# Optimization experiments

Measured on AMD Instinct MI355X. Metric: run time of the kernel, lower is better.

Reference implementation:

```python
import jax, jax.numpy as jnp
import numpy as np
import math

B, T, EMB, HD = 4, 2048, 2048, 128
HALF = HD // 2


def setup_inputs() -> dict:
    key = jax.random.key(0)
    ks = jax.random.split(key, 4)
    x = jax.random.normal(ks[0], (B, T, EMB), dtype=jnp.float32)
    s = 1.0 / math.sqrt(EMB)
    Wq = jax.random.normal(ks[1], (EMB, HD), dtype=jnp.float32) * s
    Wk = jax.random.normal(ks[2], (EMB, HD), dtype=jnp.float32) * s
    Wv = jax.random.normal(ks[3], (EMB, HD), dtype=jnp.float32) * s
    # Standard RoPE rotation table: theta_i = 10000^(-2i/HD), angle = pos * theta
    inv_freq = 1.0 / (10000.0 ** (np.arange(0, HALF, dtype=np.float32) / HALF))
    angles = np.arange(T, dtype=np.float32)[:, None] * inv_freq[None, :]  # [T, HALF]
    rot_cos = jnp.asarray(np.cos(angles), dtype=jnp.float32)
    rot_sin = jnp.asarray(np.sin(angles), dtype=jnp.float32)
    # Additive causal mask: 0 on/below diagonal, -1e9 above
    NEG = -1e9
    mask = jnp.where(jnp.tril(jnp.ones((T, T), dtype=bool)), 0.0, NEG).astype(jnp.float32)
    return {"x": x, "Wq": Wq, "Wk": Wk, "Wv": Wv,
            "rot_cos": rot_cos, "rot_sin": rot_sin, "mask": mask}


def _apply_rope(q, rot_cos, rot_sin):
    # q: [B, T, HD]; view last dim as HALF complex pairs and rotate
    qp = q.reshape(q.shape[0], q.shape[1], HALF, 2)
    re, im = qp[..., 0], qp[..., 1]
    out_re = re * rot_cos - im * rot_sin  # broadcast [T,HALF] over batch
    out_im = re * rot_sin + im * rot_cos
    return jnp.stack([out_re, out_im], axis=-1).reshape(q.shape)


def reference(x, Wq, Wk, Wv, rot_cos, rot_sin, mask):
    Q = x @ Wq  # [B, T, HD]
    K = x @ Wk
    V = x @ Wv
    Q = _apply_rope(Q, rot_cos, rot_sin)
    K = _apply_rope(K, rot_cos, rot_sin)
    scores = jnp.einsum('bqd,bkd->bqk', Q, K) / math.sqrt(HD)
    probs = jax.nn.softmax(scores + mask, axis=-1)  # dropout is identity in eval
    return jnp.einsum('bqk,bkd->bqd', probs, V)
```

## Files before the change

kernel.cpp:

```cpp
#include <hip/hip_runtime.h>
#include <cstddef>
#include <cstdint>

#define T_SEQ 2048
#define EMB_D 2048
#define HD_D  128

typedef __attribute__((ext_vector_type(8))) short short8;
typedef __attribute__((ext_vector_type(4))) float f32x4;
typedef __attribute__((ext_vector_type(4))) unsigned short ushort4v;
typedef __attribute__((ext_vector_type(8))) unsigned short ushort8v;
typedef __attribute__((ext_vector_type(2))) unsigned int uint2v;

static __device__ __forceinline__ unsigned short f2bf_rne(float f) {
    union { float f; unsigned u; } v; v.f = f;
    unsigned r = v.u + 0x7fffu + ((v.u >> 16) & 1u);
    return (unsigned short)(r >> 16);
}
static __device__ __forceinline__ unsigned short f2bf_fast(float f) {
    union { float f; unsigned u; } v; v.f = f;
    return (unsigned short)((v.u + 0x8000u) >> 16);
}
static __device__ __forceinline__ float bf2f(unsigned short h) {
    union { unsigned u; float f; } v; v.u = ((unsigned)h) << 16;
    return v.f;
}
static __device__ __forceinline__ unsigned pk2(float a, float b) {
    union { float f; unsigned u; } x, y; x.f = a; y.f = b;
    return __builtin_amdgcn_perm(y.u + 0x8000u, x.u + 0x8000u, 0x07060302);
}
#define EXP2F(x) __builtin_amdgcn_exp2f(x)

__global__ __launch_bounds__(256) void prep_weights(
    const float* __restrict__ Wq, const float* __restrict__ Wk,
    const float* __restrict__ Wv, unsigned short* __restrict__ Wt)
{
    __shared__ __attribute__((aligned(16))) unsigned short tw[64 * 132];
    const int w = blockIdx.y;
    const int k0 = blockIdx.x * 64;
    const float* W = (w == 0) ? Wq : (w == 1) ? Wk : Wv;
    const int tid = threadIdx.x;
#pragma unroll
    for (int p = 0; p < 8; p++) {
        const int f = p * 256 + tid;
        const int row = f >> 5, c4 = f & 31;
        const float4 v = *(const float4*)&W[(size_t)(k0 + row) * HD_D + c4 * 4];
        ushort4v h = { f2bf_rne(v.x), f2bf_rne(v.y), f2bf_rne(v.z), f2bf_rne(v.w) };
        *(ushort4v*)&tw[row * 132 + c4 * 4] = h;
    }
    __syncthreads();
    const int kk = (tid & 7) * 8;
#pragma unroll
    for (int p = 0; p < 4; p++) {
        const int n = p * 32 + (tid >> 3);
        ushort8v o;
#pragma unroll
        for (int jj = 0; jj < 8; jj++) o[jj] = tw[(kk + jj) * 132 + n];
        *(ushort8v*)&Wt[(size_t)w * (HD_D * EMB_D) + (size_t)n * EMB_D + k0 + kk] = o;
    }
}

__global__ __launch_bounds__(512, 4) void qkv_fused(
    const float* __restrict__ x, const unsigned short* __restrict__ Wt,
    const float* __restrict__ rcos, const float* __restrict__ rsin,
    unsigned short* __restrict__ Qb, unsigned short* __restrict__ Kb,
    unsigned short* __restrict__ Vt)
{
    __shared__ __attribute__((aligned(16))) unsigned short xsm[2][32 * 64];
    __shared__ __attribute__((aligned(16))) unsigned short wsm[2][192 * 64];
    const int L = blockIdx.x;
    const int xcd = L & 7, s = L >> 3;
    const int cg = s & 1;
    const int m0 = (xcd * 32 + (s >> 1)) * 32;
    const int tid = threadIdx.x;
    const int lane = tid & 63, wave = tid >> 6;
    const int wm = wave >> 2, wn = wave & 3;
    const int l15 = lane & 15, lq = lane >> 4;

    const int xrow = tid >> 4, xc = tid & 15;
    const float* xsrc = x + (size_t)(m0 + xrow) * EMB_D + xc * 4;
    const int wrow = tid >> 3, wc = tid & 7;
    const unsigned short* wsrc = Wt + (size_t)(cg * 192 + wrow) * EMB_D + wc * 8;

    const int xw  = xrow * 128 + (((xc >> 1) ^ (xrow & 7)) << 4) + (xc & 1) * 8;
    const int wwo = wrow * 128 + ((wc ^ (wrow & 7)) << 4);

    int ra[2], rb[3][2];
#pragma unroll
    for (int ks = 0; ks < 2; ks++) {
        const int row = wm * 16 + l15;
        ra[ks] = row * 128 + (((ks * 4 + lq) ^ (row & 7)) << 4);
    }
#pragma unroll
    for (int jj = 0; jj < 3; jj++)
#pragma unroll
        for (int ks = 0; ks < 2; ks++) {
            const int row = wn * 48 + jj * 16 + l15;
            rb[jj][ks] = row * 128 + (((ks * 4 + lq) ^ (row & 7)) << 4);
        }

    f32x4 acc[3];
#pragma unroll
    for (int j = 0; j < 3; j++) acc[j] = (f32x4){0.f, 0.f, 0.f, 0.f};

    float4 xr[3];
    short8 wr[3][3];

#define LOADN(SET, K)                                                             \
    do {                                                                          \
        xr[SET] = *(const float4*)(xsrc + (K));                                   \
        _Pragma("unroll")                                                         \
        for (int p = 0; p < 3; p++)                                               \
            wr[SET][p] = *(const short8*)(wsrc + (size_t)p * (64 * EMB_D) + (K)); \
    } while (0)

#define STAGE(SET, BUF)                                                           \
    do {                                                                          \
        char* xb = (char*)&xsm[BUF][0];                                           \
        char* wb = (char*)&wsm[BUF][0];                                           \
        uint2v u;                                                                 \
        u.x = pk2(xr[SET].x, xr[SET].y);                                          \
        u.y = pk2(xr[SET].z, xr[SET].w);                                          \
        *(uint2v*)(xb + xw) = u;                                                  \
        _Pragma("unroll")                                                         \
        for (int p = 0; p < 3; p++)                                               \
            *(short8*)(wb + wwo + p * 8192) = wr[SET][p];                         \
    } while (0)

#define COMPUTE(BUF)                                                              \
    do {                                                                          \
        const char* xb = (const char*)&xsm[BUF][0];                               \
        const char* wb = (const char*)&wsm[BUF][0];                               \
        short8 Af[2];                                                             \
        _Pragma("unroll")                                                         \
        for (int ks = 0; ks < 2; ks++)                                            \
            Af[ks] = *(const short8*)(xb + ra[ks]);                               \
        __builtin_amdgcn_s_setprio(1);                                            \
        _Pragma("unroll")                                                         \
        for (int ks = 0; ks < 2; ks++)                                            \
            _Pragma("unroll")                                                     \
            for (int jj = 0; jj < 3; jj++) {                                      \
                const short8 Bf = *(const short8*)(wb + rb[jj][ks]);              \
                acc[jj] = __builtin_amdgcn_mfma_f32_16x16x32_bf16(                \
                    Af[ks], Bf, acc[jj], 0, 0, 0);                                \
            }                                                                     \
        __builtin_amdgcn_s_setprio(0);                                            \
    } while (0)

#define BARX() asm volatile("s_waitcnt lgkmcnt(0)\n\ts_barrier" ::: "memory")

    LOADN(0, 0);
    LOADN(1, 64);
    LOADN(2, 128);
    STAGE(0, 0);
    LOADN(0, 192);

#pragma clang loop unroll(disable)
    for (int j = 0; j < 24; j += 6) {
        BARX(); STAGE(1, 1); LOADN(1, (j + 4) * 64); COMPUTE(0);
        BARX(); STAGE(2, 0); LOADN(2, (j + 5) * 64); COMPUTE(1);
        BARX(); STAGE(0, 1); LOADN(0, (j + 6) * 64); COMPUTE(0);
        BARX(); STAGE(1, 0); LOADN(1, (j + 7) * 64); COMPUTE(1);
        BARX(); STAGE(2, 1); LOADN(2, (j + 8) * 64); COMPUTE(0);
        BARX(); STAGE(0, 0); LOADN(0, (j + 9) * 64); COMPUTE(1);
    }
    BARX(); STAGE(1, 1); LOADN(1, 28 * 64); COMPUTE(0);
    BARX(); STAGE(2, 0); LOADN(2, 29 * 64); COMPUTE(1);
    BARX(); STAGE(0, 1); LOADN(0, 30 * 64); COMPUTE(0);
    BARX(); STAGE(1, 0); LOADN(1, 31 * 64); COMPUTE(1);
    BARX(); STAGE(2, 1);                    COMPUTE(0);
    BARX(); STAGE(0, 0);                    COMPUTE(1);
    BARX(); STAGE(1, 1);                    COMPUTE(0);
    BARX();                                 COMPUTE(1);

#undef LOADN
#undef STAGE
#undef COMPUTE
#undef BARX

    const float qscale = 0.08838834764831845f * 1.4426950408889634f;
#pragma unroll
    for (int r = 0; r < 4; r++) {
        const int row = m0 + wm * 16 + lq * 4 + r;
        const int t = row & (T_SEQ - 1);
        const int bb = row >> 11;
#pragma unroll
        for (int j = 0; j < 3; j++) {
            const int col = cg * 192 + wn * 48 + j * 16 + l15;
            const int mat = col >> 7, mcol = col & 127;
            const float v = acc[j][r];
            if (mat == 2) {
                Vt[((size_t)bb * HD_D + mcol) * T_SEQ + t] = f2bf_rne(v);
            } else {
                const int ip = mcol >> 1;
                const float c = rcos[t * 64 + ip];
                const float s2 = rsin[t * 64 + ip];
                const float pv = __shfl_xor(v, 1);
                float rv = (mcol & 1) ? (pv * s2 + v * c) : (v * c - pv * s2);
                if (mat == 0) {
                    rv *= qscale;
                    Qb[(size_t)row * HD_D + mcol] = f2bf_rne(rv);
                } else {
                    Kb[(size_t)row * HD_D + mcol] = f2bf_rne(rv);
                }
            }
        }
    }
}

__global__ __launch_bounds__(256, 2) void attn(
    const unsigned short* __restrict__ Qb, const unsigned short* __restrict__ Kb,
    const unsigned short* __restrict__ Vt, float* __restrict__ O0,
    unsigned short* __restrict__ O1, float* __restrict__ Lp)
{
    __shared__ __attribute__((aligned(16))) unsigned short O_s[4][32 * 128];
    __shared__ __attribute__((aligned(16))) unsigned short P_s[4][32 * 40];
    __shared__ float l_s[4][32];

    const int tid = threadIdx.x;
    const int lane = tid & 63, wave = tid >> 6;
    const int l15 = lane & 15, lq = lane >> 4;
    const int kf = lq * 8;

    const int L = blockIdx.x;
    const int g = L & 1;
    const int b = (L >> 1) & 3;
    const int q0 = (63 - (L >> 3)) * 32;
    const int kend = q0 + 32;
    const float M2 = 16.0f;

    const unsigned short* Qp = Qb + (size_t)(b * T_SEQ + q0) * HD_D;
    short8 aQ[2][4];
#pragma unroll
    for (int i = 0; i < 2; i++)
#pragma unroll
        for (int d = 0; d < 4; d++)
            aQ[i][d] = *(const short8*)&Qp[(size_t)(i * 16 + l15) * HD_D + d * 32 + kf];

    f32x4 acc[2][8];
#pragma unroll
    for (int i = 0; i < 2; i++)
#pragma unroll
        for (int d = 0; d < 8; d++) acc[i][d] = (f32x4){0.f, 0.f, 0.f, 0.f};
    float l_r[2][4] = {{0.f, 0.f, 0.f, 0.f}, {0.f, 0.f, 0.f, 0.f}};

    const unsigned short* Kbase = Kb + (size_t)b * T_SEQ * HD_D;
    const unsigned short* Vbase = Vt + (size_t)b * HD_D * T_SEQ;
    unsigned short* Pw = &P_s[wave][0];

    for (int c = 2 * wave + g; c * 32 < kend; c += 8) {
        const int kA = c * 32;
        const unsigned short* Kp = Kbase + (size_t)kA * HD_D;
        short8 KA[8];
#pragma unroll
        for (int d = 0; d < 4; d++)
#pragma unroll
            for (int n = 0; n < 2; n++)
                KA[d * 2 + n] = *(const short8*)&Kp[(size_t)(n * 16 + l15) * HD_D + d * 32 + kf];

        f32x4 sc[2][2];
#pragma unroll
        for (int i = 0; i < 2; i++)
#pragma unroll
            for (int n = 0; n < 2; n++) sc[i][n] = (f32x4){0.f, 0.f, 0.f, 0.f};
#pragma unroll
        for (int d = 0; d < 4; d++)
#pragma unroll
            for (int i = 0; i < 2; i++)
#pragma unroll
                for (int n = 0; n < 2; n++)
                    sc[i][n] = __builtin_amdgcn_mfma_f32_16x16x32_bf16(
                        aQ[i][d], KA[d * 2 + n], sc[i][n], 0, 0, 0);

        short8 VA[8];
#pragma unroll
        for (int d = 0; d < 8; d++)
            VA[d] = *(const short8*)&Vbase[(size_t)(d * 16 + l15) * T_SEQ + kA + kf];

#pragma unroll
        for (int i = 0; i < 2; i++)
#pragma unroll
            for (int r = 0; r < 4; r++) {
                const int q = q0 + i * 16 + lq * 4 + r;
                const float p0 = ((kA + l15)      <= q) ? EXP2F(sc[i][0][r] - M2) : 0.f;
                const float p1 = ((kA + 16 + l15) <= q) ? EXP2F(sc[i][1][r] - M2) : 0.f;
                l_r[i][r] += p0 + p1;
                const int prow = (i * 16 + lq * 4 + r) * 40;
                Pw[prow + l15]      = f2bf_fast(p0);
                Pw[prow + 16 + l15] = f2bf_fast(p1);
            }
        short8 pA[2];
#pragma unroll
        for (int i = 0; i < 2; i++)
            pA[i] = *(const short8*)&Pw[(i * 16 + l15) * 40 + kf];
#pragma unroll
        for (int i = 0; i < 2; i++)
#pragma unroll
            for (int d = 0; d < 8; d++)
                acc[i][d] = __builtin_amdgcn_mfma_f32_16x16x32_bf16(pA[i], VA[d], acc[i][d], 0, 0, 0);
    }

#pragma unroll
    for (int i = 0; i < 2; i++)
#pragma unroll
        for (int r = 0; r < 4; r++) {
            float lr = l_r[i][r];
            lr += __shfl_xor(lr, 1);
            lr += __shfl_xor(lr, 2);
            lr += __shfl_xor(lr, 4);
            lr += __shfl_xor(lr, 8);
            if (l15 == 0) l_s[wave][i * 16 + lq * 4 + r] = lr;
#pragma unroll
            for (int d = 0; d < 8; d++)
                O_s[wave][(i * 16 + lq * 4 + r) * 128 + d * 16 + l15] = f2bf_fast(acc[i][d][r]);
        }
    __syncthreads();

#pragma unroll
    for (int pass = 0; pass < 2; pass++) {
        const int row = pass * 16 + (tid >> 4);
        const int dc = (tid & 15) * 8;
        const float lt = l_s[0][row] + l_s[1][row] + l_s[2][row] + l_s[3][row];
        float o[8];
#pragma unroll
        for (int k = 0; k < 8; k++) o[k] = 0.f;
#pragma unroll
        for (int w2 = 0; w2 < 4; w2++) {
            const ushort8v pv = *(const ushort8v*)&O_s[w2][row * 128 + dc];
#pragma unroll
            for (int k = 0; k < 8; k++) o[k] += bf2f(pv[k]);
        }
        const size_t grow = (size_t)(b * T_SEQ + q0 + row);
        if (g == 0) {
            float* op = O0 + grow * HD_D + dc;
#pragma unroll
            for (int k = 0; k < 8; k++) op[k] = o[k];
        } else {
            ushort8v h;
#pragma unroll
            for (int k = 0; k < 8; k++) h[k] = f2bf_fast(o[k]);
            *(ushort8v*)&O1[grow * HD_D + dc] = h;
        }
        if ((tid & 15) == 0) Lp[g * 8192 + grow] = lt;
    }
}

__global__ __launch_bounds__(256) void attn_merge(
    float* __restrict__ out, const unsigned short* __restrict__ O1,
    const float* __restrict__ Lp)
{
    const int idx = blockIdx.x * 256 + threadIdx.x;
    const int row = idx >> 5;
    f32x4 a = ((f32x4*)out)[idx];
    const ushort4v h = ((const ushort4v*)O1)[idx];
    f32x4 bv = { bf2f(h.x), bf2f(h.y), bf2f(h.z), bf2f(h.w) };
    const float inv = 1.0f / (Lp[row] + Lp[8192 + row]);
    ((f32x4*)out)[idx] = (a + bv) * inv;
}

extern "C" void kernel_launch(void* const* d_in, const int* in_sizes, int n_in,
                              void* d_out, int out_size, void* d_ws, size_t ws_size,
                              hipStream_t stream)
{
    (void)in_sizes; (void)n_in; (void)out_size; (void)ws_size;
    const float* x  = (const float*)d_in[0];
    const float* Wq = (const float*)d_in[1];
    const float* Wk = (const float*)d_in[2];
    const float* Wv = (const float*)d_in[3];
    const float* rc = (const float*)d_in[4];
    const float* rs = (const float*)d_in[5];
    float* out = (float*)d_out;

    char* ws = (char*)d_ws;
    unsigned short* Wt = (unsigned short*)(ws);
    unsigned short* Qb = (unsigned short*)(ws + 1572864);
    unsigned short* Kb = (unsigned short*)(ws + 3670016);
    unsigned short* Vt = (unsigned short*)(ws + 5767168);
    unsigned short* O1 = (unsigned short*)(ws + 7864320);
    float*          Lp = (float*)(ws + 9961472);

    prep_weights<<<dim3(32, 3), 256, 0, stream>>>(Wq, Wk, Wv, Wt);
    qkv_fused   <<<dim3(512),   512, 0, stream>>>(x, Wt, rc, rs, Qb, Kb, Vt);
    attn        <<<dim3(512),   256, 0, stream>>>(Qb, Kb, Vt, out, O1, Lp);
    attn_merge  <<<dim3(1024),  256, 0, stream>>>(out, O1, Lp);
}
```

Measured before the change: 173.5 us.

## Retile QKV projection to 64x96 block tiles with 128-wide K steps

The QKV projection now gives each block a 64-row by 96-column output tile (four column groups) instead of 32x192. Each of 4 waves computes 2x3 MFMA tiles, and the K step grows from 64 to 128, with double buffering replacing the triple-register pipeline. The aim is more MFMA work per LDS fragment load (A fragments reused across three B tiles, B across two A tiles) and fewer barriers. In exchange it uses more registers, fewer waves per block, and larger LDS use, which may lower occupancy.

```diff
diff --git a/kernel.cpp b/kernel.cpp
--- a/kernel.cpp
+++ b/kernel.cpp
@@ -60,148 +60,162 @@
     }
 }
 
-__global__ __launch_bounds__(512, 4) void qkv_fused(
+__global__ __launch_bounds__(256, 2) void qkv_fused(
     const float* __restrict__ x, const unsigned short* __restrict__ Wt,
     const float* __restrict__ rcos, const float* __restrict__ rsin,
     unsigned short* __restrict__ Qb, unsigned short* __restrict__ Kb,
     unsigned short* __restrict__ Vt)
 {
-    __shared__ __attribute__((aligned(16))) unsigned short xsm[2][32 * 64];
-    __shared__ __attribute__((aligned(16))) unsigned short wsm[2][192 * 64];
+    __shared__ __attribute__((aligned(16))) unsigned short xsm[2][64 * 128];
+    __shared__ __attribute__((aligned(16))) unsigned short wsm[2][96 * 128];
     const int L = blockIdx.x;
     const int xcd = L & 7, s = L >> 3;
-    const int cg = s & 1;
-    const int m0 = (xcd * 32 + (s >> 1)) * 32;
+    const int ng = s & 3;
+    const int m0 = (xcd * 16 + (s >> 2)) * 64;
     const int tid = threadIdx.x;
     const int lane = tid & 63, wave = tid >> 6;
-    const int wm = wave >> 2, wn = wave & 3;
+    const int wm = wave >> 1, wn = wave & 1;
     const int l15 = lane & 15, lq = lane >> 4;
 
-    const int xrow = tid >> 4, xc = tid & 15;
-    const float* xsrc = x + (size_t)(m0 + xrow) * EMB_D + xc * 4;
-    const int wrow = tid >> 3, wc = tid & 7;
-    const unsigned short* wsrc = Wt + (size_t)(cg * 192 + wrow) * EMB_D + wc * 8;
-
-    const int xw  = xrow * 128 + (((xc >> 1) ^ (xrow & 7)) << 4) + (xc & 1) * 8;
-    const int wwo = wrow * 128 + ((wc ^ (wrow & 7)) << 4);
-
-    int ra[2], rb[3][2];
-#pragma unroll
-    for (int ks = 0; ks < 2; ks++) {
-        const int row = wm * 16 + l15;
-        ra[ks] = row * 128 + (((ks * 4 + lq) ^ (row & 7)) << 4);
-    }
+    const int xrow = tid >> 5, xc4 = tid & 31;
+    const float* xsrc = x + (size_t)(m0 + xrow) * EMB_D + xc4 * 4;
+    const int wrow = tid >> 4, wc = tid & 15;
+    const unsigned short* wsrc = Wt + (size_t)(ng * 96 + wrow) * EMB_D + wc * 8;
+
+    const int xw  = xrow * 256 + (((xc4 >> 1) ^ (xrow & 7)) << 4) + (xc4 & 1) * 8;
+    const int wwo = wrow * 256 + ((wc ^ (wrow & 7)) << 4);
+
+    int ra[2][4], rb[3][4];
+#pragma unroll
+    for (int i = 0; i < 2; i++)
+#pragma unroll
+        for (int ks = 0; ks < 4; ks++) {
+            const int row = wm * 32 + i * 16 + l15;
+            ra[i][ks] = row * 256 + (((ks * 4 + lq) ^ (row & 7)) << 4);
+        }
 #pragma unroll
     for (int jj = 0; jj < 3; jj++)
 #pragma unroll
-        for (int ks = 0; ks < 2; ks++) {
+        for (int ks = 0; ks < 4; ks++) {
             const int row = wn * 48 + jj * 16 + l15;
-            rb[jj][ks] = row * 128 + (((ks * 4 + lq) ^ (row & 7)) << 4);
-        }
-
-    f32x4 acc[3];
-#pragma unroll
-    for (int j = 0; j < 3; j++) acc[j] = (f32x4){0.f, 0.f, 0.f, 0.f};
-
-    float4 xr[3];
-    short8 wr[3][3];
-
-#define LOADN(SET, K)                                                             \
-    do {                                                                          \
-        xr[SET] = *(const float4*)(xsrc + (K));                                   \
-        _Pragma("unroll")                                                         \
-        for (int p = 0; p < 3; p++)                                               \
-            wr[SET][p] = *(const short8*)(wsrc + (size_t)p * (64 * EMB_D) + (K)); \
+            rb[jj][ks] = row * 256 + (((ks * 4 + lq) ^ (row & 7)) << 4);
+        }
+
+    f32x4 acc[2][3];
+#pragma unroll
+    for (int i = 0; i < 2; i++)
+#pragma unroll
+        for (int j = 0; j < 3; j++) acc[i][j] = (f32x4){0.f, 0.f, 0.f, 0.f};
+
+    float4 xr[2][8];
+    short8 wr[6];
+
+#define LOADX(S, K)                                                              \
+    do {                                                                         \
+        _Pragma("unroll")                                                        \
+        for (int p = 0; p < 8; p++)                                              \
+            xr[S][p] = *(const float4*)(xsrc + (size_t)p * (8 * EMB_D) + (K));   \
     } while (0)
 
-#define STAGE(SET, BUF)                                                           \
-    do {                                                                          \
-        char* xb = (char*)&xsm[BUF][0];                                           \
-        char* wb = (char*)&wsm[BUF][0];                                           \
-        uint2v u;                                                                 \
-        u.x = pk2(xr[SET].x, xr[SET].y);                                          \
-        u.y = pk2(xr[SET].z, xr[SET].w);                                          \
-        *(uint2v*)(xb + xw) = u;                                                  \
-        _Pragma("unroll")                                                         \
-        for (int p = 0; p < 3; p++)                                               \
-            *(short8*)(wb + wwo + p * 8192) = wr[SET][p];                         \
+#define LOADW(K)                                                                 \
+    do {                                                                         \
+        _Pragma("unroll")                                                        \
+        for (int p = 0; p < 6; p++)                                              \
+            wr[p] = *(const short8*)(wsrc + (size_t)p * (16 * EMB_D) + (K));     \
     } while (0)
 
-#define COMPUTE(BUF)                                                              \
-    do {                                                                          \
-        const char* xb = (const char*)&xsm[BUF][0];                               \
-        const char* wb = (const char*)&wsm[BUF][0];                               \
-        short8 Af[2];                                                             \
-        _Pragma("unroll")                                                         \
-        for (int ks = 0; ks < 2; ks++)                                            \
-            Af[ks] = *(const short8*)(xb + ra[ks]);                               \
-        __builtin_amdgcn_s_setprio(1);                                            \
-        _Pragma("unroll")                                                         \
-        for (int ks = 0; ks < 2; ks++)                                            \
-            _Pragma("unroll")                                                     \
-            for (int jj = 0; jj < 3; jj++) {                                      \
-                const short8 Bf = *(const short8*)(wb + rb[jj][ks]);              \
-                acc[jj] = __builtin_amdgcn_mfma_f32_16x16x32_bf16(                \
-                    Af[ks], Bf, acc[jj], 0, 0, 0);                                \
-            }                                                                     \
-        __builtin_amdgcn_s_setprio(0);                                            \
+#define STAGE(S, BUF)                                                            \
+    do {                                                                         \
+        char* xb = (char*)&xsm[BUF][0];                                          \
+        char* wb = (char*)&wsm[BUF][0];                                          \
+        _Pragma("unroll")                                                        \
+        for (int p = 0; p < 8; p++) {                                            \
+            uint2v u;                                                            \
+            u.x = pk2(xr[S][p].x, xr[S][p].y);                                   \
+            u.y = pk2(xr[S][p].z, xr[S][p].w);                                   \
+            *(uint2v*)(xb + xw + p * 2048) = u;                                  \
+        }                                                                        \
+        _Pragma("unroll")                                                        \
+        for (int p = 0; p < 6; p++)                                              \
+            *(short8*)(wb + wwo + p * 4096) = wr[p];                             \
     } while (0)
 
+#define COMPUTE(BUF)                                                             \
+    do {                                                                         \
+        const char* xb = (const char*)&xsm[BUF][0];                              \
+        const char* wb = (const char*)&wsm[BUF][0];                              \
+        short8 Af[2][4];                                                         \
+        _Pragma("unroll")                                                        \
+        for (int i = 0; i < 2; i++)                                              \
+            _Pragma("unroll")                                                    \
+            for (int ks = 0; ks < 4; ks++)                                       \
+                Af[i][ks] = *(const short8*)(xb + ra[i][ks]);                     \
+        __builtin_amdgcn_s_setprio(1);                                           \
+        _Pragma("unroll")                                                        \
+        for (int ks = 0; ks < 4; ks++)                                           \
+            _Pragma("unroll")                                                    \
+            for (int jj = 0; jj < 3; jj++) {                                     \
+                const short8 Bf = *(const short8*)(wb + rb[jj][ks]);             \
+                _Pragma("unroll")                                                \
+                for (int i = 0; i < 2; i++)                                      \
+                    acc[i][jj] = __builtin_amdgcn_mfma_f32_16x16x32_bf16(        \
+                        Af[i][ks], Bf, acc[i][jj], 0, 0, 0);                     \
+            }                                                                    \
+        __builtin_amdgcn_s_setprio(0);                                           \
+    } while (0)
+
 #define BARX() asm volatile("s_waitcnt lgkmcnt(0)\n\ts_barrier" ::: "memory")
 
-    LOADN(0, 0);
-    LOADN(1, 64);
-    LOADN(2, 128);
+    LOADX(0, 0);
+    LOADW(0);
+    LOADX(1, 128);
     STAGE(0, 0);
-    LOADN(0, 192);
+    LOADW(128);
+    LOADX(0, 256);
 
 #pragma clang loop unroll(disable)
-    for (int j = 0; j < 24; j += 6) {
-        BARX(); STAGE(1, 1); LOADN(1, (j + 4) * 64); COMPUTE(0);
-        BARX(); STAGE(2, 0); LOADN(2, (j + 5) * 64); COMPUTE(1);
-        BARX(); STAGE(0, 1); LOADN(0, (j + 6) * 64); COMPUTE(0);
-        BARX(); STAGE(1, 0); LOADN(1, (j + 7) * 64); COMPUTE(1);
-        BARX(); STAGE(2, 1); LOADN(2, (j + 8) * 64); COMPUTE(0);
-        BARX(); STAGE(0, 0); LOADN(0, (j + 9) * 64); COMPUTE(1);
-    }
-    BARX(); STAGE(1, 1); LOADN(1, 28 * 64); COMPUTE(0);
-    BARX(); STAGE(2, 0); LOADN(2, 29 * 64); COMPUTE(1);
-    BARX(); STAGE(0, 1); LOADN(0, 30 * 64); COMPUTE(0);
-    BARX(); STAGE(1, 0); LOADN(1, 31 * 64); COMPUTE(1);
-    BARX(); STAGE(2, 1);                    COMPUTE(0);
-    BARX(); STAGE(0, 0);                    COMPUTE(1);
-    BARX(); STAGE(1, 1);                    COMPUTE(0);
-    BARX();                                 COMPUTE(1);
-
-#undef LOADN
+    for (int j = 0; j < 12; j += 2) {
+        BARX(); STAGE(1, 1); LOADW((j + 2) * 128); LOADX(1, (j + 3) * 128); COMPUTE(0);
+        BARX(); STAGE(0, 0); LOADW((j + 3) * 128); LOADX(0, (j + 4) * 128); COMPUTE(1);
+    }
+    BARX(); STAGE(1, 1); LOADW(14 * 128); LOADX(1, 15 * 128); COMPUTE(0);
+    BARX(); STAGE(0, 0); LOADW(15 * 128);                     COMPUTE(1);
+    BARX(); STAGE(1, 1);                                      COMPUTE(0);
+    BARX();                                                   COMPUTE(1);
+
+#undef LOADX
+#undef LOADW
 #undef STAGE
 #undef COMPUTE
 #undef BARX
 
     const float qscale = 0.08838834764831845f * 1.4426950408889634f;
 #pragma unroll
-    for (int r = 0; r < 4; r++) {
-        const int row = m0 + wm * 16 + lq * 4 + r;
-        const int t = row & (T_SEQ - 1);
-        const int bb = row >> 11;
-#pragma unroll
-        for (int j = 0; j < 3; j++) {
-            const int col = cg * 192 + wn * 48 + j * 16 + l15;
-            const int mat = col >> 7, mcol = col & 127;
-            const float v = acc[j][r];
-            if (mat == 2) {
-                Vt[((size_t)bb * HD_D + mcol) * T_SEQ + t] = f2bf_rne(v);
-            } else {
-                const int ip = mcol >> 1;
-                const float c = rcos[t * 64 + ip];
-                const float s2 = rsin[t * 64 + ip];
-                const float pv = __shfl_xor(v, 1);
-                float rv = (mcol & 1) ? (pv * s2 + v * c) : (v * c - pv * s2);
-                if (mat == 0) {
-                    rv *= qscale;
-                    Qb[(size_t)row * HD_D + mcol] = f2bf_rne(rv);
+    for (int i = 0; i < 2; i++) {
+#pragma unroll
+        for (int r = 0; r < 4; r++) {
+            const int row = m0 + wm * 32 + i * 16 + lq * 4 + r;
+            const int t = row & (T_SEQ - 1);
+            const int bb = row >> 11;
+#pragma unroll
+            for (int j = 0; j < 3; j++) {
+                const int col = ng * 96 + wn * 48 + j * 16 + l15;
+                const int mat = col >> 7, mcol = col & 127;
+                const float v = acc[i][j][r];
+                if (mat == 2) {
+                    Vt[((size_t)bb * HD_D + mcol) * T_SEQ + t] = f2bf_rne(v);
                 } else {
-                    Kb[(size_t)row * HD_D + mcol] = f2bf_rne(rv);
+                    const int ip = mcol >> 1;
+                    const float c = rcos[t * 64 + ip];
+                    const float s2 = rsin[t * 64 + ip];
+                    const float pv = __shfl_xor(v, 1);
+                    float rv = (mcol & 1) ? (pv * s2 + v * c) : (v * c - pv * s2);
+                    if (mat == 0) {
+                        rv *= qscale;
+                        Qb[(size_t)row * HD_D + mcol] = f2bf_rne(rv);
+                    } else {
+                        Kb[(size_t)row * HD_D + mcol] = f2bf_rne(rv);
+                    }
                 }
             }
         }
@@ -380,7 +394,7 @@
     float*          Lp = (float*)(ws + 9961472);
 
     prep_weights<<<dim3(32, 3), 256, 0, stream>>>(Wq, Wk, Wv, Wt);
-    qkv_fused   <<<dim3(512),   512, 0, stream>>>(x, Wt, rc, rs, Qb, Kb, Vt);
+    qkv_fused   <<<dim3(512),   256, 0, stream>>>(x, Wt, rc, rs, Qb, Kb, Vt);
     attn        <<<dim3(512),   256, 0, stream>>>(Qb, Kb, Vt, out, O1, Lp);
     attn_merge  <<<dim3(1024),  256, 0, stream>>>(out, O1, Lp);
 }
```

Result: no change. 171.7 us (-1.1%).

## Load QKV weight fragments directly from global into registers, drop W LDS staging

Applied to the files above, without the earlier changes.

The QKV projection kernel now gives each block a 16-row tile spanning all 384 output columns, instead of a 32-row by 192-column tile. Each wave loads its weight B-fragments directly from global memory into registers, and only x is staged through LDS, with a K step of 128. This removes the LDS traffic and footprint for the weight tile and halves the number of barrier steps. In exchange, each weight element is re-read from global/L2 by every block with no reuse across waves, and the smaller M tile means more blocks each re-fetching all of W.

```diff
diff --git a/kernel.cpp b/kernel.cpp
--- a/kernel.cpp
+++ b/kernel.cpp
@@ -66,114 +66,90 @@
     unsigned short* __restrict__ Qb, unsigned short* __restrict__ Kb,
     unsigned short* __restrict__ Vt)
 {
-    __shared__ __attribute__((aligned(16))) unsigned short xsm[2][32 * 64];
-    __shared__ __attribute__((aligned(16))) unsigned short wsm[2][192 * 64];
+    __shared__ __attribute__((aligned(16))) unsigned short xsm[2][16 * 128];
     const int L = blockIdx.x;
-    const int xcd = L & 7, s = L >> 3;
-    const int cg = s & 1;
-    const int m0 = (xcd * 32 + (s >> 1)) * 32;
+    const int m0 = ((L & 7) * 64 + (L >> 3)) * 16;
     const int tid = threadIdx.x;
-    const int lane = tid & 63, wave = tid >> 6;
-    const int wm = wave >> 2, wn = wave & 3;
+    const int lane = tid & 63, wn = tid >> 6;
     const int l15 = lane & 15, lq = lane >> 4;
 
-    const int xrow = tid >> 4, xc = tid & 15;
-    const float* xsrc = x + (size_t)(m0 + xrow) * EMB_D + xc * 4;
-    const int wrow = tid >> 3, wc = tid & 7;
-    const unsigned short* wsrc = Wt + (size_t)(cg * 192 + wrow) * EMB_D + wc * 8;
-
-    const int xw  = xrow * 128 + (((xc >> 1) ^ (xrow & 7)) << 4) + (xc & 1) * 8;
-    const int wwo = wrow * 128 + ((wc ^ (wrow & 7)) << 4);
-
-    int ra[2], rb[3][2];
-#pragma unroll
-    for (int ks = 0; ks < 2; ks++) {
-        const int row = wm * 16 + l15;
-        ra[ks] = row * 128 + (((ks * 4 + lq) ^ (row & 7)) << 4);
-    }
+    const int xrow = tid >> 5, xc4 = tid & 31;
+    const float* xsrc = x + (size_t)(m0 + xrow) * EMB_D + xc4 * 4;
+    const int xw = xrow * 256 + (((xc4 >> 1) ^ (xrow & 7)) << 4) + (xc4 & 1) * 8;
+
+    int ra[4];
+#pragma unroll
+    for (int ks = 0; ks < 4; ks++)
+        ra[ks] = l15 * 256 + (((ks * 4 + lq) ^ (l15 & 7)) << 4);
+
+    const unsigned short* wptr[3];
 #pragma unroll
     for (int jj = 0; jj < 3; jj++)
-#pragma unroll
-        for (int ks = 0; ks < 2; ks++) {
-            const int row = wn * 48 + jj * 16 + l15;
-            rb[jj][ks] = row * 128 + (((ks * 4 + lq) ^ (row & 7)) << 4);
-        }
+        wptr[jj] = Wt + (size_t)(wn * 48 + jj * 16 + l15) * EMB_D + lq * 8;
 
     f32x4 acc[3];
 #pragma unroll
     for (int j = 0; j < 3; j++) acc[j] = (f32x4){0.f, 0.f, 0.f, 0.f};
 
-    float4 xr[3];
-    short8 wr[3][3];
-
-#define LOADN(SET, K)                                                             \
-    do {                                                                          \
-        xr[SET] = *(const float4*)(xsrc + (K));                                   \
-        _Pragma("unroll")                                                         \
-        for (int p = 0; p < 3; p++)                                               \
-            wr[SET][p] = *(const short8*)(wsrc + (size_t)p * (64 * EMB_D) + (K)); \
+    float4 xr[2];
+    short8 wr[3][4];
+
+#define LOADX(S, K) do { xr[S] = *(const float4*)(xsrc + (K)); } while (0)
+
+#define LOADW(K)                                                               \
+    do {                                                                       \
+        _Pragma("unroll")                                                      \
+        for (int jj = 0; jj < 3; jj++)                                         \
+            _Pragma("unroll")                                                  \
+            for (int ks = 0; ks < 4; ks++)                                     \
+                wr[jj][ks] = *(const short8*)(wptr[jj] + (K) + ks * 32);       \
     } while (0)
 
-#define STAGE(SET, BUF)                                                           \
-    do {                                                                          \
-        char* xb = (char*)&xsm[BUF][0];                                           \
-        char* wb = (char*)&wsm[BUF][0];                                           \
-        uint2v u;                                                                 \
-        u.x = pk2(xr[SET].x, xr[SET].y);                                          \
-        u.y = pk2(xr[SET].z, xr[SET].w);                                          \
-        *(uint2v*)(xb + xw) = u;                                                  \
-        _Pragma("unroll")                                                         \
-        for (int p = 0; p < 3; p++)                                               \
-            *(short8*)(wb + wwo + p * 8192) = wr[SET][p];                         \
+#define STAGE(S, BUF)                                                          \
+    do {                                                                       \
+        uint2v u;                                                              \
+        u.x = pk2(xr[S].x, xr[S].y);                                           \
+        u.y = pk2(xr[S].z, xr[S].w);                                           \
+        *(uint2v*)((char*)&xsm[BUF][0] + xw) = u;                              \
     } while (0)
 
-#define COMPUTE(BUF)                                                              \
-    do {                                                                          \
-        const char* xb = (const char*)&xsm[BUF][0];                               \
-        const char* wb = (const char*)&wsm[BUF][0];                               \
-        short8 Af[2];                                                             \
-        _Pragma("unroll")                                                         \
-        for (int ks = 0; ks < 2; ks++)                                            \
-            Af[ks] = *(const short8*)(xb + ra[ks]);                               \
-        __builtin_amdgcn_s_setprio(1);                                            \
-        _Pragma("unroll")                                                         \
-        for (int ks = 0; ks < 2; ks++)                                            \
-            _Pragma("unroll")                                                     \
-            for (int jj = 0; jj < 3; jj++) {                                      \
-                const short8 Bf = *(const short8*)(wb + rb[jj][ks]);              \
-                acc[jj] = __builtin_amdgcn_mfma_f32_16x16x32_bf16(                \
-                    Af[ks], Bf, acc[jj], 0, 0, 0);                                \
-            }                                                                     \
-        __builtin_amdgcn_s_setprio(0);                                            \
+#define COMPUTE(BUF)                                                           \
+    do {                                                                       \
+        const char* xb = (const char*)&xsm[BUF][0];                            \
+        short8 Af[4];                                                          \
+        _Pragma("unroll")                                                      \
+        for (int ks = 0; ks < 4; ks++)                                         \
+            Af[ks] = *(const short8*)(xb + ra[ks]);                            \
+        __builtin_amdgcn_s_setprio(1);                                         \
+        _Pragma("unroll")                                                      \
+        for (int ks = 0; ks < 4; ks++)                                         \
+            _Pragma("unroll")                                                  \
+            for (int jj = 0; jj < 3; jj++)                                     \
+                acc[jj] = __builtin_amdgcn_mfma_f32_16x16x32_bf16(             \
+                    Af[ks], wr[jj][ks], acc[jj], 0, 0, 0);                     \
+        __builtin_amdgcn_s_setprio(0);                                         \
     } while (0)
 
 #define BARX() asm volatile("s_waitcnt lgkmcnt(0)\n\ts_barrier" ::: "memory")
 
-    LOADN(0, 0);
-    LOADN(1, 64);
-    LOADN(2, 128);
+    LOADX(0, 0);
+    LOADW(0);
+    LOADX(1, 128);
     STAGE(0, 0);
-    LOADN(0, 192);
+    LOADX(0, 256);
 
 #pragma clang loop unroll(disable)
-    for (int j = 0; j < 24; j += 6) {
-        BARX(); STAGE(1, 1); LOADN(1, (j + 4) * 64); COMPUTE(0);
-        BARX(); STAGE(2, 0); LOADN(2, (j + 5) * 64); COMPUTE(1);
-        BARX(); STAGE(0, 1); LOADN(0, (j + 6) * 64); COMPUTE(0);
-        BARX(); STAGE(1, 0); LOADN(1, (j + 7) * 64); COMPUTE(1);
-        BARX(); STAGE(2, 1); LOADN(2, (j + 8) * 64); COMPUTE(0);
-        BARX(); STAGE(0, 0); LOADN(0, (j + 9) * 64); COMPUTE(1);
-    }
-    BARX(); STAGE(1, 1); LOADN(1, 28 * 64); COMPUTE(0);
-    BARX(); STAGE(2, 0); LOADN(2, 29 * 64); COMPUTE(1);
-    BARX(); STAGE(0, 1); LOADN(0, 30 * 64); COMPUTE(0);
-    BARX(); STAGE(1, 0); LOADN(1, 31 * 64); COMPUTE(1);
-    BARX(); STAGE(2, 1);                    COMPUTE(0);
-    BARX(); STAGE(0, 0);                    COMPUTE(1);
-    BARX(); STAGE(1, 1);                    COMPUTE(0);
-    BARX();                                 COMPUTE(1);
-
-#undef LOADN
+    for (int j = 0; j < 12; j += 2) {
+        BARX(); STAGE(1, 1); LOADX(1, (j + 3) * 128); COMPUTE(0); LOADW((j + 1) * 128);
+        BARX(); STAGE(0, 0); LOADX(0, (j + 4) * 128); COMPUTE(1); LOADW((j + 2) * 128);
+    }
+    BARX(); STAGE(1, 1); LOADX(1, 15 * 128); COMPUTE(0); LOADW(13 * 128);
+    BARX(); STAGE(0, 0);                     COMPUTE(1); LOADW(14 * 128);
+    BARX(); STAGE(1, 1);                     COMPUTE(0); LOADW(15 * 128);
+    BARX();                                  COMPUTE(1);
+
+#undef LOADX
+#undef LOADW
 #undef STAGE
 #undef COMPUTE
 #undef BARX
@@ -181,12 +157,12 @@
     const float qscale = 0.08838834764831845f * 1.4426950408889634f;
 #pragma unroll
     for (int r = 0; r < 4; r++) {
-        const int row = m0 + wm * 16 + lq * 4 + r;
+        const int row = m0 + lq * 4 + r;
         const int t = row & (T_SEQ - 1);
         const int bb = row >> 11;
 #pragma unroll
         for (int j = 0; j < 3; j++) {
-            const int col = cg * 192 + wn * 48 + j * 16 + l15;
+            const int col = wn * 48 + j * 16 + l15;
             const int mat = col >> 7, mcol = col & 127;
             const float v = acc[j][r];
             if (mat == 2) {
```

Measured after the change: 223.7 us. +28.9%, slower.
